# Kernel tuning notes

Measured on AMD Instinct MI355X. Metric: run time of the kernel, lower is better.

## Reference

```python
import jax, jax.numpy as jnp
import numpy as np

B, S, HID = 1, 2048, 4096
NH, NKV = 32, 8
HD = HID // NH            # 128
GROUPS = NH // NKV        # 4
ROPE_THETA = 10000.0


def _rope_cos_sin(seq_len, head_dim, dtype=jnp.float32):
    inv_freq = 1.0 / (ROPE_THETA ** (jnp.arange(0, head_dim, 2, dtype=jnp.float32) / head_dim))
    t = jnp.arange(seq_len, dtype=jnp.float32)
    freqs = jnp.outer(t, inv_freq)                      # [S, HD/2]
    emb = jnp.concatenate([freqs, freqs], axis=-1)      # [S, HD]
    return jnp.cos(emb).astype(dtype), jnp.sin(emb).astype(dtype)


def _rotate_half(x):
    x1, x2 = jnp.split(x, 2, axis=-1)
    return jnp.concatenate([-x2, x1], axis=-1)


def _apply_rope(x, cos, sin):
    # x: [B, H, S, HD]; cos/sin: [S, HD] (position_ids = arange(S), no past)
    return x * cos[None, None] + _rotate_half(x) * sin[None, None]


def setup_inputs() -> dict:
    key = jax.random.key(0)
    k1, k2, k3, k4, k5 = jax.random.split(key, 5)
    return {
        "hidden_states": jax.random.normal(k1, (B, S, HID), jnp.float32),
        "Wq": jax.random.normal(k2, (NH * HD, HID), jnp.float32) * 0.02,
        "Wk": jax.random.normal(k3, (NKV * HD, HID), jnp.float32) * 0.02,
        "Wv": jax.random.normal(k4, (NKV * HD, HID), jnp.float32) * 0.02,
        "Wo": jax.random.normal(k5, (HID, NH * HD), jnp.float32) * 0.02,
    }


def reference(hidden_states, Wq, Wk, Wv, Wo):
    bsz, q_len, _ = hidden_states.shape
    # projections (nn.Linear: x @ W.T)
    q = (hidden_states @ Wq.T).reshape(bsz, q_len, NH, HD).transpose(0, 2, 1, 3)   # [B,NH,S,HD]
    k = (hidden_states @ Wk.T).reshape(bsz, q_len, NKV, HD).transpose(0, 2, 1, 3)  # [B,NKV,S,HD]
    v = (hidden_states @ Wv.T).reshape(bsz, q_len, NKV, HD).transpose(0, 2, 1, 3)

    cos, sin = _rope_cos_sin(q_len, HD, hidden_states.dtype)
    q = _apply_rope(q, cos, sin)
    k = _apply_rope(k, cos, sin)

    # GQA: repeat kv heads (repeat_kv / num_key_value_groups)
    k = jnp.repeat(k, GROUPS, axis=1)   # [B,NH,S,HD]
    v = jnp.repeat(v, GROUPS, axis=1)

    scale = 1.0 / jnp.sqrt(jnp.asarray(HD, hidden_states.dtype))
    logits = jnp.einsum('bhqd,bhkd->bhqk', q, k) * scale   # [B,NH,S,S]

    # prefill causal mask (phys_past_len = 0)
    causal = jnp.tril(jnp.ones((q_len, q_len), dtype=bool))
    logits = jnp.where(causal[None, None], logits, jnp.finfo(logits.dtype).min)

    attn = jax.nn.softmax(logits, axis=-1)
    out = jnp.einsum('bhqk,bhkd->bhqd', attn, v)            # [B,NH,S,HD]
    out = out.transpose(0, 2, 1, 3).reshape(bsz, q_len, NH * HD)
    return out @ Wo.T
```

## Files before the change

### kernel.cpp

```cpp
#include <hip/hip_runtime.h>

typedef __bf16 bf16;
typedef __bf16 bf16x2 __attribute__((ext_vector_type(2)));
typedef __bf16 bf16x4 __attribute__((ext_vector_type(4)));
typedef __bf16 bf16x8 __attribute__((ext_vector_type(8)));
typedef float f32x4 __attribute__((ext_vector_type(4)));

#define S_LEN 2048
#define HID_DIM 4096
#define NH 32
#define NKV 8
#define HD 128
#define QKV_N 6144
#define K_COL 4096
#define V_COL 5120
#define PADV 76

__global__ void cvt_all_kernel(const float* __restrict__ hs, const float* __restrict__ wq,
                               const float* __restrict__ wk, const float* __restrict__ wv,
                               const float* __restrict__ wo, bf16* __restrict__ hsb,
                               bf16* __restrict__ wqkvb, bf16* __restrict__ wob,
                               float* __restrict__ cost, float* __restrict__ sint) {
  long i = (long)blockIdx.x * blockDim.x + threadIdx.x;
  if (i >= 12582912) {
    int j = (int)(i - 12582912);
    int s = j >> 6, d = j & 63;
    float inv = expf(-0.14391156831212787f * (float)d);
    float ang = (float)s * inv;
    cost[j] = cosf(ang);
    sint[j] = sinf(ang);
    return;
  }
  const float* src; bf16* dst; long off;
  if (i < 2097152)      { src = hs; dst = hsb;                          off = i; }
  else if (i < 6291456) { src = wq; dst = wqkvb;                        off = i - 2097152; }
  else if (i < 7340032) { src = wk; dst = wqkvb + (long)4096 * 4096;    off = i - 6291456; }
  else if (i < 8388608) { src = wv; dst = wqkvb + (long)5120 * 4096;    off = i - 7340032; }
  else                  { src = wo; dst = wob;                          off = i - 8388608; }
  float4 v = reinterpret_cast<const float4*>(src)[off];
  bf16x4 o;
  o[0] = (bf16)v.x; o[1] = (bf16)v.y; o[2] = (bf16)v.z; o[3] = (bf16)v.w;
  reinterpret_cast<bf16x4*>(dst)[off] = o;
}

__global__ void rope_apply_kernel(bf16* __restrict__ qkv, const float* __restrict__ cost,
                                  const float* __restrict__ sint) {
  int idx = blockIdx.x * blockDim.x + threadIdx.x;
  int s = idx / 320;
  int c = idx - s * 320;
  int g = c >> 3, dc = (c & 7) * 8;
  long base = (long)s * QKV_N + g * 128 + dc;
  bf16x8 x1 = *reinterpret_cast<const bf16x8*>(qkv + base);
  bf16x8 x2 = *reinterpret_cast<const bf16x8*>(qkv + base + 64);
  const float* cp = cost + (s << 6) + dc;
  const float* sp = sint + (s << 6) + dc;
  float4 ca = *reinterpret_cast<const float4*>(cp);
  float4 cb = *reinterpret_cast<const float4*>(cp + 4);
  float4 sa = *reinterpret_cast<const float4*>(sp);
  float4 sb = *reinterpret_cast<const float4*>(sp + 4);
  float co[8] = {ca.x, ca.y, ca.z, ca.w, cb.x, cb.y, cb.z, cb.w};
  float sn[8] = {sa.x, sa.y, sa.z, sa.w, sb.x, sb.y, sb.z, sb.w};
  bf16x8 y1, y2;
#pragma unroll
  for (int e = 0; e < 8; ++e) {
    float a = (float)x1[e], b = (float)x2[e];
    y1[e] = (bf16)(a * co[e] - b * sn[e]);
    y2[e] = (bf16)(b * co[e] + a * sn[e]);
  }
  *reinterpret_cast<bf16x8*>(qkv + base)      = y1;
  *reinterpret_cast<bf16x8*>(qkv + base + 64) = y2;
}

#define STG8(buf, mat, kt, unit) {                                                       \
    const bf16* sp_ = (mat) ? Bp : Ap;                                                   \
    int row0_ = ((mat) ? n0 : m0) + (unit) * 64;                                         \
    int lb_ = (buf) * LBUF + (mat) * 16384 + (unit) * 4096;                              \
    int r_ = t >> 3, jl_ = t & 7, jg_ = jl_ ^ (r_ & 7);                                  \
    const bf16* src_ = sp_ + (long)(row0_ + r_) * K + (kt) * 64 + jg_ * 8;               \
    __builtin_amdgcn_global_load_lds((const __attribute__((address_space(1))) void*)src_,\
        (__attribute__((address_space(3))) void*)(L + lb_ + t * 8), 16, 0, 0); }

#define DSA2(buf, mh) {                                                                  \
    _Pragma("unroll") for (int ks_ = 0; ks_ < 2; ++ks_)                                  \
      _Pragma("unroll") for (int mf_ = 0; mf_ < 4; ++mf_) {                              \
        int R_ = wr * 128 + (mh) * 64 + mf_ * 16 + lm;                                   \
        aF[ks_][mf_] = *reinterpret_cast<const bf16x8*>(                                 \
            L + (buf) * LBUF + R_ * 64 + (((ks_ * 4 + lg) ^ (R_ & 7)) << 3));            \
      } }

#define DSBALL(buf) {                                                                    \
    _Pragma("unroll") for (int ks_ = 0; ks_ < 2; ++ks_)                                  \
      _Pragma("unroll") for (int nf_ = 0; nf_ < NB; ++nf_) {                             \
        int R_ = wc * (NB * 16) + nf_ * 16 + lm;                                         \
        bF[ks_][nf_] = *reinterpret_cast<const bf16x8*>(                                 \
            L + (buf) * LBUF + 16384 + R_ * 64 + (((ks_ * 4 + lg) ^ (R_ & 7)) << 3));    \
      } }

#define MM2(mh) {                                                                        \
    __builtin_amdgcn_s_setprio(1);                                                       \
    _Pragma("unroll") for (int mf_ = 0; mf_ < 4; ++mf_)                                  \
      _Pragma("unroll") for (int nf_ = 0; nf_ < NB; ++nf_)                               \
        _Pragma("unroll") for (int ks_ = 0; ks_ < 2; ++ks_)                              \
          acc[(mh) * 4 + mf_][nf_] = __builtin_amdgcn_mfma_f32_16x16x32_bf16(            \
              aF[ks_][mf_], bF[ks_][nf_], acc[(mh) * 4 + mf_][nf_], 0, 0, 0);            \
    __builtin_amdgcn_s_setprio(0); }

#define BAR() __builtin_amdgcn_s_barrier()
#define WVM(n) asm volatile("s_waitcnt vmcnt(%0)" :: "i"(n) : "memory")

template<int NB, typename OutT>
__global__ __launch_bounds__(512, 1) void gemm4p_kernel(
    const bf16* __restrict__ Ap, const bf16* __restrict__ Bp, OutT* __restrict__ C,
    int M, int N, int K) {
  constexpr int LBUF = 16384 + NB * 4096;
  __shared__ __align__(16) bf16 L[2 * LBUF];

  int nwg = gridDim.x * gridDim.y;
  int bid = blockIdx.y * gridDim.x + blockIdx.x;
  int cpx = nwg >> 3;
  int swz = (bid & 7) * cpx + (bid >> 3);
  int bxs = swz % gridDim.x, bys = swz / gridDim.x;
  const int n0 = bxs * (NB * 64), m0 = bys * 256;

  const int t = threadIdx.x;
  const int lane = t & 63, w = t >> 6;
  const int wr = w >> 2, wc = w & 3;
  const int lg = lane >> 4, lm = lane & 15;
  const int NT = K >> 6;

  f32x4 acc[8][NB] = {};
  bf16x8 aF[2][4], bF[2][NB];

  STG8(0, 0, 0, 0); STG8(0, 0, 0, 1); STG8(0, 0, 0, 2); STG8(0, 0, 0, 3);
  STG8(0, 1, 0, 0); if (NB > 1) STG8(0, 1, 0, 1); if (NB > 2) STG8(0, 1, 0, 2);
  STG8(1, 1, 1, 0); if (NB > 1) STG8(1, 1, 1, 1); if (NB > 2) STG8(1, 1, 1, 2);
  WVM(NB);
  BAR();

  for (int I = 0; I < (NT >> 1); ++I) {
    const int tt = 2 * I;
    const bool pf = (I < (NT >> 1) - 1);
    DSA2(0, 0); DSBALL(0);
    STG8(1, 0, tt + 1, 0); STG8(1, 0, tt + 1, 1);
    STG8(1, 0, tt + 1, 2); STG8(1, 0, tt + 1, 3);
    BAR(); MM2(0); BAR();
    DSA2(0, 1);
    if (pf) { STG8(0, 1, tt + 2, 0); if (NB > 1) STG8(0, 1, tt + 2, 1);
              if (NB > 2) STG8(0, 1, tt + 2, 2); }
    BAR(); MM2(1);
    if (pf) WVM(NB); else WVM(0);
    BAR();
    DSA2(1, 0); DSBALL(1);
    if (pf) { STG8(0, 0, tt + 2, 0); STG8(0, 0, tt + 2, 1);
              STG8(0, 0, tt + 2, 2); STG8(0, 0, tt + 2, 3); }
    BAR(); MM2(0); BAR();
    DSA2(1, 1);
    if (pf) { STG8(1, 1, tt + 3, 0); if (NB > 1) STG8(1, 1, tt + 3, 1);
              if (NB > 2) STG8(1, 1, tt + 3, 2); }
    BAR(); MM2(1);
    if (pf) WVM(NB); else WVM(0);
    BAR();
  }

#pragma unroll
  for (int am = 0; am < 8; ++am) {
    int row = m0 + wr * 128 + am * 16 + lg * 4;
#pragma unroll
    for (int nf = 0; nf < NB; ++nf) {
      int col = n0 + wc * (NB * 16) + nf * 16 + lm;
#pragma unroll
      for (int rr = 0; rr < 4; ++rr) {
        if constexpr (sizeof(OutT) == 4) C[(long)(row + rr) * N + col] = acc[am][nf][rr];
        else                             C[(long)(row + rr) * N + col] = (bf16)acc[am][nf][rr];
      }
    }
  }
}

__global__ __launch_bounds__(512, 4) void attn_kernel(const bf16* __restrict__ qkv,
                                                      bf16* __restrict__ out) {
  __shared__ __align__(16) bf16 Ks[2][64 * 128];
  __shared__ __align__(16) bf16 Vt[128 * PADV];

  const int bx = blockIdx.x;
  const int qt = 15 - (bx >> 5);
  const int h = bx & 31;
  const int kvh = h >> 2;
  const int q0 = qt * 128;
  const int t = threadIdx.x, lane = t & 63, w = t >> 6;
  const int lg = lane >> 4, lm = lane & 15;
  const int dchunk = t >> 5, kv2 = t & 31;
  const int kva = kv2 * 2;
  const int k5 = kva & 31;
  const int slot = ((kva >> 5) << 5) | (((k5 >> 2) & 3) << 3) | ((k5 >> 4) << 2) | (k5 & 3);
  const bf16* kbase = qkv + K_COL + kvh * HD;
  const bf16* vbase = qkv + V_COL + kvh * HD;

  const long qrow = q0 + w * 16 + lm;
  bf16x8 qf[4];
#pragma unroll
  for (int ks = 0; ks < 4; ++ks)
    qf[ks] = *reinterpret_cast<const bf16x8*>(qkv + qrow * QKV_N + h * HD + ks * 32 + lg * 8);

  f32x4 o[8];
#pragma unroll
  for (int i = 0; i < 8; ++i) o[i] = f32x4{0.f, 0.f, 0.f, 0.f};
  float mrow = -1e30f, lrow = 0.f;

  bf16x8 a0, a1;
  {
#pragma unroll
    for (int i = 0; i < 2; ++i) {
      int c = i * 512 + t;
      int r = c >> 4, jl = c & 15;
      int jg = jl ^ (r & 15);
      const bf16* src = kbase + (long)r * QKV_N + jg * 8;
      __builtin_amdgcn_global_load_lds((const __attribute__((address_space(1))) void*)src,
                                       (__attribute__((address_space(3))) void*)(Ks[0] + c * 8), 16, 0, 0);
    }
    const bf16* vs = vbase + (long)kva * QKV_N + dchunk * 8;
    a0 = *reinterpret_cast<const bf16x8*>(vs);
    a1 = *reinterpret_cast<const bf16x8*>(vs + QKV_N);
  }

  const int nst = 2 * qt + 2;
  for (int st = 0; st < nst; ++st) {
    const int cur = st & 1;
#pragma unroll
    for (int e = 0; e < 8; ++e) {
      bf16x2 pk; pk[0] = a0[e]; pk[1] = a1[e];
      *reinterpret_cast<bf16x2*>(Vt + (dchunk * 8 + e) * PADV + slot) = pk;
    }
    __syncthreads();

    if (st + 1 < nst) {
      const long kv0n = (long)(st + 1) * 64;
#pragma unroll
      for (int i = 0; i < 2; ++i) {
        int c = i * 512 + t;
        int r = c >> 4, jl = c & 15;
        int jg = jl ^ (r & 15);
        const bf16* src = kbase + (kv0n + r) * QKV_N + jg * 8;
        __builtin_amdgcn_global_load_lds((const __attribute__((address_space(1))) void*)src,
                                         (__attribute__((address_space(3))) void*)(Ks[cur ^ 1] + c * 8), 16, 0, 0);
      }
      const bf16* vs = vbase + (kv0n + kva) * QKV_N + dchunk * 8;
      a0 = *reinterpret_cast<const bf16x8*>(vs);
      a1 = *reinterpret_cast<const bf16x8*>(vs + QKV_N);
    }

    const int kv0 = st * 64;
    const int qg = q0 + w * 16 + lm;
    if (kv0 <= q0 + w * 16 + 15) {
      f32x4 s[4];
#pragma unroll
      for (int cb = 0; cb < 4; ++cb) s[cb] = f32x4{0.f, 0.f, 0.f, 0.f};
      __builtin_amdgcn_s_setprio(1);
#pragma unroll
      for (int ks = 0; ks < 4; ++ks) {
#pragma unroll
        for (int cb = 0; cb < 4; ++cb) {
          bf16x8 kf = *reinterpret_cast<const bf16x8*>(
              Ks[cur] + (cb * 16 + lm) * 128 + (((ks * 4 + lg) ^ lm) << 3));
          s[cb] = __builtin_amdgcn_mfma_f32_16x16x32_bf16(kf, qf[ks], s[cb], 0, 0, 0);
        }
      }
      __builtin_amdgcn_s_setprio(0);

      const float SC = 0.12751742f;
      float sl[4][4];
#pragma unroll
      for (int cb = 0; cb < 4; ++cb)
#pragma unroll
        for (int r = 0; r < 4; ++r) {
          float v = s[cb][r] * SC;
          if (st >= nst - 2 && (kv0 + cb * 16 + lg * 4 + r) > qg) v = -1e30f;
          sl[cb][r] = v;
        }
      float tm = sl[0][0];
#pragma unroll
      for (int cb = 0; cb < 4; ++cb)
#pragma unroll
        for (int r = 0; r < 4; ++r) tm = fmaxf(tm, sl[cb][r]);
      tm = fmaxf(tm, __shfl_xor(tm, 16));
      tm = fmaxf(tm, __shfl_xor(tm, 32));

      if (__any(tm > mrow + 8.f)) {
        float mnew = fmaxf(mrow, tm);
        float alpha = exp2f(mrow - mnew);
        mrow = mnew;
        lrow *= alpha;
        float ar[4];
#pragma unroll
        for (int r = 0; r < 4; ++r)
          ar[r] = __shfl(alpha, (lane & 48) | (lg * 4 + r));
#pragma unroll
        for (int i = 0; i < 8; ++i)
#pragma unroll
          for (int r = 0; r < 4; ++r) o[i][r] *= ar[r];
      }
      float p[4][4];
      float psum = 0.f;
#pragma unroll
      for (int cb = 0; cb < 4; ++cb)
#pragma unroll
        for (int r = 0; r < 4; ++r) {
          p[cb][r] = exp2f(sl[cb][r] - mrow);
          psum += p[cb][r];
        }
      psum += __shfl_xor(psum, 16);
      psum += __shfl_xor(psum, 32);
      lrow += psum;

      bf16x8 pa0, pa1;
#pragma unroll
      for (int r = 0; r < 4; ++r) {
        pa0[r]     = (bf16)p[0][r];
        pa0[4 + r] = (bf16)p[1][r];
        pa1[r]     = (bf16)p[2][r];
        pa1[4 + r] = (bf16)p[3][r];
      }

      __builtin_amdgcn_s_setprio(1);
#pragma unroll
      for (int db = 0; db < 8; ++db) {
        bf16x8 vf0 = *reinterpret_cast<const bf16x8*>(Vt + (db * 16 + lm) * PADV + lg * 8);
        bf16x8 vf1 = *reinterpret_cast<const bf16x8*>(Vt + (db * 16 + lm) * PADV + 32 + lg * 8);
        o[db] = __builtin_amdgcn_mfma_f32_16x16x32_bf16(pa0, vf0, o[db], 0, 0, 0);
        o[db] = __builtin_amdgcn_mfma_f32_16x16x32_bf16(pa1, vf1, o[db], 0, 0, 0);
      }
      __builtin_amdgcn_s_setprio(0);
    }

    if (st + 1 < nst) __syncthreads();
  }

  float invr[4];
#pragma unroll
  for (int r = 0; r < 4; ++r)
    invr[r] = 1.0f / __shfl(lrow, (lane & 48) | (lg * 4 + r));
#pragma unroll
  for (int r = 0; r < 4; ++r) {
    long row = q0 + w * 16 + lg * 4 + r;
#pragma unroll
    for (int db = 0; db < 8; ++db)
      out[row * HID_DIM + h * HD + db * 16 + lm] = (bf16)(o[db][r] * invr[r]);
  }
}

extern "C" void kernel_launch(void* const* d_in, const int* in_sizes, int n_in,
                              void* d_out, int out_size, void* d_ws, size_t ws_size,
                              hipStream_t stream) {
  const float* hs = (const float*)d_in[0];
  const float* Wq = (const float*)d_in[1];
  const float* Wk = (const float*)d_in[2];
  const float* Wv = (const float*)d_in[3];
  const float* Wo = (const float*)d_in[4];
  float* out = (float*)d_out;
  char* ws = (char*)d_ws;

  bf16*  hsb   = (bf16*)(ws);
  bf16*  wqkvb = (bf16*)(ws + 16777216);
  bf16*  wob   = (bf16*)(ws + 67108864);
  bf16*  qkv   = (bf16*)(ws + 100663296);
  bf16*  attn  = (bf16*)(ws + 125829120);
  float* cost  = (float*)(ws + 142606336);
  float* sint  = (float*)(ws + 143130624);

  cvt_all_kernel<<<49664, 256, 0, stream>>>(hs, Wq, Wk, Wv, Wo, hsb, wqkvb, wob, cost, sint);
  gemm4p_kernel<3, bf16><<<dim3(32, 8), 512, 0, stream>>>(hsb, wqkvb, qkv, 2048, 6144, 4096);
  rope_apply_kernel<<<2560, 256, 0, stream>>>(qkv, cost, sint);
  attn_kernel<<<512, 512, 0, stream>>>(qkv, attn);
  gemm4p_kernel<2, float><<<dim3(32, 8), 512, 0, stream>>>(attn, wob, out, 2048, 4096, 4096);
}
```

Measured before the change: 309.2 us.

## Deepen attention K/V prefetch pipeline with manual unroll and vmcnt barriers

```diff
diff --git a/kernel.cpp b/kernel.cpp
--- a/kernel.cpp
+++ b/kernel.cpp
@@ -177,6 +177,95 @@
   }
 }
 
+#define AK_LBAR() { asm volatile("s_waitcnt lgkmcnt(0)" ::: "memory");                   \
+                    __builtin_amdgcn_s_barrier(); }
+#define AK_VBAR() { asm volatile("s_waitcnt vmcnt(4)" ::: "memory");                     \
+                    __builtin_amdgcn_sched_barrier(0);                                   \
+                    asm volatile("s_waitcnt lgkmcnt(0)" ::: "memory");                   \
+                    __builtin_amdgcn_s_barrier(); }
+
+#define AK_WRITEV(r0, r1) {                                                              \
+    _Pragma("unroll") for (int e = 0; e < 8; ++e) {                                      \
+      bf16x2 pk; pk[0] = r0[e]; pk[1] = r1[e];                                           \
+      *reinterpret_cast<bf16x2*>(Vt + (dchunk * 8 + e) * PADV + slot) = pk;              \
+    } }
+
+#define AK_ISSUEV(base, r0, r1) {                                                        \
+    long rv_ = (long)(base) + kva; if (rv_ > 2046) rv_ = 2046;                           \
+    const bf16* vs_ = vbase + rv_ * QKV_N + dchunk * 8;                                  \
+    r0 = *reinterpret_cast<const bf16x8*>(vs_);                                          \
+    r1 = *reinterpret_cast<const bf16x8*>(vs_ + QKV_N); }
+
+#define AK_ISSUEK(base, buf) {                                                           \
+    _Pragma("unroll") for (int i_ = 0; i_ < 2; ++i_) {                                   \
+      int c_ = i_ * 512 + t;                                                             \
+      int r_ = c_ >> 4, jl_ = c_ & 15, jg_ = jl_ ^ (r_ & 15);                            \
+      long rk_ = (long)(base) + r_; if (rk_ > 2047) rk_ = 2047;                          \
+      const bf16* src_ = kbase + rk_ * QKV_N + jg_ * 8;                                  \
+      __builtin_amdgcn_global_load_lds((const __attribute__((address_space(1))) void*)src_,\
+          (__attribute__((address_space(3))) void*)(Ks[buf] + c_ * 8), 16, 0, 0);        \
+    } }
+
+#define AK_STEP(stv, ksb) {                                                              \
+    const int st_ = (stv);                                                               \
+    const int kv0_ = st_ * 64;                                                           \
+    if (kv0_ <= q0 + w * 16 + 15) {                                                      \
+      f32x4 s[4];                                                                        \
+      _Pragma("unroll") for (int cb = 0; cb < 4; ++cb) s[cb] = f32x4{0.f,0.f,0.f,0.f};   \
+      __builtin_amdgcn_s_setprio(1);                                                     \
+      _Pragma("unroll") for (int ks = 0; ks < 4; ++ks)                                   \
+        _Pragma("unroll") for (int cb = 0; cb < 4; ++cb) {                               \
+          bf16x8 kf = *reinterpret_cast<const bf16x8*>(                                  \
+              Ks[ksb] + (cb * 16 + lm) * 128 + (((ks * 4 + lg) ^ lm) << 3));             \
+          s[cb] = __builtin_amdgcn_mfma_f32_16x16x32_bf16(kf, qf[ks], s[cb], 0, 0, 0);   \
+        }                                                                                \
+      __builtin_amdgcn_s_setprio(0);                                                     \
+      const float SC = 0.12751742f;                                                      \
+      float sl[4][4];                                                                    \
+      _Pragma("unroll") for (int cb = 0; cb < 4; ++cb)                                   \
+        _Pragma("unroll") for (int r = 0; r < 4; ++r) {                                  \
+          float v = s[cb][r] * SC;                                                       \
+          if (st_ >= nst - 2 && (kv0_ + cb * 16 + lg * 4 + r) > qg) v = -1e30f;          \
+          sl[cb][r] = v;                                                                 \
+        }                                                                                \
+      float tm = sl[0][0];                                                               \
+      _Pragma("unroll") for (int cb = 0; cb < 4; ++cb)                                   \
+        _Pragma("unroll") for (int r = 0; r < 4; ++r) tm = fmaxf(tm, sl[cb][r]);         \
+      tm = fmaxf(tm, __shfl_xor(tm, 16));                                                \
+      tm = fmaxf(tm, __shfl_xor(tm, 32));                                                \
+      if (__any(tm > mrow + 8.f)) {                                                      \
+        float mnew = fmaxf(mrow, tm);                                                    \
+        float alpha = exp2f(mrow - mnew);                                                \
+        mrow = mnew; lrow *= alpha;                                                      \
+        float ar[4];                                                                     \
+        _Pragma("unroll") for (int r = 0; r < 4; ++r)                                    \
+          ar[r] = __shfl(alpha, (lane & 48) | (lg * 4 + r));                             \
+        _Pragma("unroll") for (int i = 0; i < 8; ++i)                                    \
+          _Pragma("unroll") for (int r = 0; r < 4; ++r) o[i][r] *= ar[r];                \
+      }                                                                                  \
+      float p[4][4]; float psum = 0.f;                                                   \
+      _Pragma("unroll") for (int cb = 0; cb < 4; ++cb)                                   \
+        _Pragma("unroll") for (int r = 0; r < 4; ++r) {                                  \
+          p[cb][r] = exp2f(sl[cb][r] - mrow); psum += p[cb][r];                          \
+        }                                                                                \
+      psum += __shfl_xor(psum, 16);                                                      \
+      psum += __shfl_xor(psum, 32);                                                      \
+      lrow += psum;                                                                      \
+      bf16x8 pa0, pa1;                                                                   \
+      _Pragma("unroll") for (int r = 0; r < 4; ++r) {                                    \
+        pa0[r] = (bf16)p[0][r]; pa0[4 + r] = (bf16)p[1][r];                              \
+        pa1[r] = (bf16)p[2][r]; pa1[4 + r] = (bf16)p[3][r];                              \
+      }                                                                                  \
+      __builtin_amdgcn_s_setprio(1);                                                     \
+      _Pragma("unroll") for (int db = 0; db < 8; ++db) {                                 \
+        bf16x8 vf0 = *reinterpret_cast<const bf16x8*>(Vt + (db*16+lm)*PADV + lg*8);      \
+        bf16x8 vf1 = *reinterpret_cast<const bf16x8*>(Vt + (db*16+lm)*PADV + 32 + lg*8); \
+        o[db] = __builtin_amdgcn_mfma_f32_16x16x32_bf16(pa0, vf0, o[db], 0, 0, 0);       \
+        o[db] = __builtin_amdgcn_mfma_f32_16x16x32_bf16(pa1, vf1, o[db], 0, 0, 0);       \
+      }                                                                                  \
+      __builtin_amdgcn_s_setprio(0);                                                     \
+    } }
+
 __global__ __launch_bounds__(512, 4) void attn_kernel(const bf16* __restrict__ qkv,
                                                       bf16* __restrict__ out) {
   __shared__ __align__(16) bf16 Ks[2][64 * 128];
@@ -197,6 +286,7 @@
   const bf16* vbase = qkv + V_COL + kvh * HD;
 
   const long qrow = q0 + w * 16 + lm;
+  const int qg = q0 + w * 16 + lm;
   bf16x8 qf[4];
 #pragma unroll
   for (int ks = 0; ks < 4; ++ks)
@@ -207,132 +297,30 @@
   for (int i = 0; i < 8; ++i) o[i] = f32x4{0.f, 0.f, 0.f, 0.f};
   float mrow = -1e30f, lrow = 0.f;
 
-  bf16x8 a0, a1;
-  {
-#pragma unroll
-    for (int i = 0; i < 2; ++i) {
-      int c = i * 512 + t;
-      int r = c >> 4, jl = c & 15;
-      int jg = jl ^ (r & 15);
-      const bf16* src = kbase + (long)r * QKV_N + jg * 8;
-      __builtin_amdgcn_global_load_lds((const __attribute__((address_space(1))) void*)src,
-                                       (__attribute__((address_space(3))) void*)(Ks[0] + c * 8), 16, 0, 0);
-    }
-    const bf16* vs = vbase + (long)kva * QKV_N + dchunk * 8;
-    a0 = *reinterpret_cast<const bf16x8*>(vs);
-    a1 = *reinterpret_cast<const bf16x8*>(vs + QKV_N);
-  }
-
   const int nst = 2 * qt + 2;
-  for (int st = 0; st < nst; ++st) {
-    const int cur = st & 1;
-#pragma unroll
-    for (int e = 0; e < 8; ++e) {
-      bf16x2 pk; pk[0] = a0[e]; pk[1] = a1[e];
-      *reinterpret_cast<bf16x2*>(Vt + (dchunk * 8 + e) * PADV + slot) = pk;
-    }
-    __syncthreads();
-
-    if (st + 1 < nst) {
-      const long kv0n = (long)(st + 1) * 64;
-#pragma unroll
-      for (int i = 0; i < 2; ++i) {
-        int c = i * 512 + t;
-        int r = c >> 4, jl = c & 15;
-        int jg = jl ^ (r & 15);
-        const bf16* src = kbase + (kv0n + r) * QKV_N + jg * 8;
-        __builtin_amdgcn_global_load_lds((const __attribute__((address_space(1))) void*)src,
-                                         (__attribute__((address_space(3))) void*)(Ks[cur ^ 1] + c * 8), 16, 0, 0);
-      }
-      const bf16* vs = vbase + (kv0n + kva) * QKV_N + dchunk * 8;
-      a0 = *reinterpret_cast<const bf16x8*>(vs);
-      a1 = *reinterpret_cast<const bf16x8*>(vs + QKV_N);
-    }
-
-    const int kv0 = st * 64;
-    const int qg = q0 + w * 16 + lm;
-    if (kv0 <= q0 + w * 16 + 15) {
-      f32x4 s[4];
-#pragma unroll
-      for (int cb = 0; cb < 4; ++cb) s[cb] = f32x4{0.f, 0.f, 0.f, 0.f};
-      __builtin_amdgcn_s_setprio(1);
-#pragma unroll
-      for (int ks = 0; ks < 4; ++ks) {
-#pragma unroll
-        for (int cb = 0; cb < 4; ++cb) {
-          bf16x8 kf = *reinterpret_cast<const bf16x8*>(
-              Ks[cur] + (cb * 16 + lm) * 128 + (((ks * 4 + lg) ^ lm) << 3));
-          s[cb] = __builtin_amdgcn_mfma_f32_16x16x32_bf16(kf, qf[ks], s[cb], 0, 0, 0);
-        }
-      }
-      __builtin_amdgcn_s_setprio(0);
-
-      const float SC = 0.12751742f;
-      float sl[4][4];
-#pragma unroll
-      for (int cb = 0; cb < 4; ++cb)
-#pragma unroll
-        for (int r = 0; r < 4; ++r) {
-          float v = s[cb][r] * SC;
-          if (st >= nst - 2 && (kv0 + cb * 16 + lg * 4 + r) > qg) v = -1e30f;
-          sl[cb][r] = v;
-        }
-      float tm = sl[0][0];
-#pragma unroll
-      for (int cb = 0; cb < 4; ++cb)
-#pragma unroll
-        for (int r = 0; r < 4; ++r) tm = fmaxf(tm, sl[cb][r]);
-      tm = fmaxf(tm, __shfl_xor(tm, 16));
-      tm = fmaxf(tm, __shfl_xor(tm, 32));
-
-      if (__any(tm > mrow + 8.f)) {
-        float mnew = fmaxf(mrow, tm);
-        float alpha = exp2f(mrow - mnew);
-        mrow = mnew;
-        lrow *= alpha;
-        float ar[4];
-#pragma unroll
-        for (int r = 0; r < 4; ++r)
-          ar[r] = __shfl(alpha, (lane & 48) | (lg * 4 + r));
-#pragma unroll
-        for (int i = 0; i < 8; ++i)
-#pragma unroll
-          for (int r = 0; r < 4; ++r) o[i][r] *= ar[r];
-      }
-      float p[4][4];
-      float psum = 0.f;
-#pragma unroll
-      for (int cb = 0; cb < 4; ++cb)
-#pragma unroll
-        for (int r = 0; r < 4; ++r) {
-          p[cb][r] = exp2f(sl[cb][r] - mrow);
-          psum += p[cb][r];
-        }
-      psum += __shfl_xor(psum, 16);
-      psum += __shfl_xor(psum, 32);
-      lrow += psum;
-
-      bf16x8 pa0, pa1;
-#pragma unroll
-      for (int r = 0; r < 4; ++r) {
-        pa0[r]     = (bf16)p[0][r];
-        pa0[4 + r] = (bf16)p[1][r];
-        pa1[r]     = (bf16)p[2][r];
-        pa1[4 + r] = (bf16)p[3][r];
-      }
-
-      __builtin_amdgcn_s_setprio(1);
-#pragma unroll
-      for (int db = 0; db < 8; ++db) {
-        bf16x8 vf0 = *reinterpret_cast<const bf16x8*>(Vt + (db * 16 + lm) * PADV + lg * 8);
-        bf16x8 vf1 = *reinterpret_cast<const bf16x8*>(Vt + (db * 16 + lm) * PADV + 32 + lg * 8);
-        o[db] = __builtin_amdgcn_mfma_f32_16x16x32_bf16(pa0, vf0, o[db], 0, 0, 0);
-        o[db] = __builtin_amdgcn_mfma_f32_16x16x32_bf16(pa1, vf1, o[db], 0, 0, 0);
-      }
-      __builtin_amdgcn_s_setprio(0);
-    }
-
-    if (st + 1 < nst) __syncthreads();
+  bf16x8 va0, va1, vb0, vb1;
+
+  AK_ISSUEV(0, va0, va1);
+  AK_ISSUEK(0, 0);
+  AK_ISSUEV(64, vb0, vb1);
+  AK_ISSUEK(64, 1);
+  AK_WRITEV(va0, va1);
+  AK_VBAR();
+
+  for (int I = 0; I < (nst >> 1); ++I) {
+    const int s0 = 2 * I;
+    AK_STEP(s0, 0);
+    AK_LBAR();
+    AK_WRITEV(vb0, vb1);
+    AK_ISSUEV((s0 + 2) * 64, va0, va1);
+    AK_ISSUEK((s0 + 2) * 64, 0);
+    AK_VBAR();
+    AK_STEP(s0 + 1, 1);
+    AK_LBAR();
+    AK_WRITEV(va0, va1);
+    AK_ISSUEV((s0 + 3) * 64, vb0, vb1);
+    AK_ISSUEK((s0 + 3) * 64, 1);
+    AK_VBAR();
   }
 
   float invr[4];
```

Measured after the change: 302.5 us. -2.2%, faster.
